# Kernel optimization log

Measured on AMD Instinct MI355X. Metric: run time of the kernel, lower is better.

Reference implementation:

```python
import jax, jax.numpy as jnp
import numpy as np

M, N, E, IN, C, HID, TOPK = 4, 50000, 400000, 128, 128, 256, 2
NEG_SLOPE = 0.2


def setup_inputs() -> dict:
    key = jax.random.key(0)
    k = jax.random.split(key, 16)
    s = lambda f: 1.0 / np.sqrt(f)
    return {
        "x_src": jax.random.normal(k[0], (M, N, IN), jnp.float32),
        "x_dst": jax.random.normal(k[1], (N, IN), jnp.float32),
        "src_idx": jax.random.randint(k[2], (M, E), 0, N),
        "dst_idx": jax.random.randint(k[3], (M, E), 0, N),
        "proj_Ws": jax.random.normal(k[4], (M, IN, C), jnp.float32) * s(IN),
        "proj_bs": jnp.zeros((M, C), jnp.float32),
        "projd_W": jax.random.normal(k[5], (IN, C), jnp.float32) * s(IN),
        "projd_b": jnp.zeros((C,), jnp.float32),
        "lin_src": jax.random.normal(k[6], (M, C), jnp.float32) * s(C),
        "lin_dst": jax.random.normal(k[7], (M, C), jnp.float32) * s(C),
        "gm_W1": jax.random.normal(k[8], (C, C), jnp.float32) * s(C),
        "gm_b1": jnp.zeros((C,), jnp.float32),
        "gm_W2": jax.random.normal(k[9], (C, C), jnp.float32) * s(C),
        "gm_b2": jnp.zeros((C,), jnp.float32),
        "gate_W1": jax.random.normal(k[10], (M * C, HID), jnp.float32) * s(M * C),
        "gate_b1": jnp.zeros((HID,), jnp.float32),
        "gate_W2": jax.random.normal(k[11], (HID, M), jnp.float32) * s(HID),
        "gate_b2": jnp.zeros((M,), jnp.float32),
        "exp_W1": jax.random.normal(k[12], (M, C, HID), jnp.float32) * s(C),
        "exp_b1": jnp.zeros((M, HID), jnp.float32),
        "exp_W2": jax.random.normal(k[13], (M, HID, C), jnp.float32) * s(HID),
        "exp_b2": jnp.zeros((M, C), jnp.float32),
    }


def _propagate(xs_t, asrc_t, adst_t, si, di, recept_t):
    # GAT-style attention message passing for one edge type.
    # xs_t: [N,C] projected src feats, asrc_t/adst_t: [N] attn logits,
    # si/di: [E] edge endpoints, recept_t: [N] per-dst-node receptivity gate.
    e = jax.nn.leaky_relu(asrc_t[si] + adst_t[di], NEG_SLOPE)  # [E]
    emax = jax.ops.segment_max(e, di, num_segments=N)
    ez = jnp.exp(e - emax[di])
    den = jax.ops.segment_sum(ez, di, num_segments=N)
    alpha = ez / (den[di] + 1e-16)                             # softmax per dst node
    msg = xs_t[si] * (alpha * recept_t[di])[:, None]           # [E,C]
    return jax.ops.segment_sum(msg, di, num_segments=N)       # [N,C]


def reference(x_src, x_dst, src_idx, dst_idx, proj_Ws, proj_bs, projd_W, projd_b,
              lin_src, lin_dst, gm_W1, gm_b1, gm_W2, gm_b2,
              gate_W1, gate_b1, gate_W2, gate_b2,
              exp_W1, exp_b1, exp_W2, exp_b2):
    # --- SynapticConvLayer (eval path, heads=1) ---
    xs = jnp.einsum('mni,mic->mnc', x_src, proj_Ws) + proj_bs[:, None, :]  # [M,N,C]
    xd = x_dst @ projd_W + projd_b                                          # [N,C]
    a_src = jnp.einsum('mnc,mc->mn', xs, lin_src)
    a_dst = jnp.einsum('nc,mc->mn', xd[None].repeat(M, 0) * 0 + xd[None], lin_dst) if False else jnp.einsum('nc,mc->mn', xd, lin_dst)
    prop = jax.vmap(_propagate)
    out1 = prop(xs, a_src, a_dst, src_idx, dst_idx, jnp.ones((M, N), xs.dtype))
    # receptivity from grad_map surrogate (inference branch)
    feat_diff = out1 - xd[None]                                            # [M,N,C]
    mo = jax.nn.sigmoid(jax.nn.relu(feat_diff @ gm_W1 + gm_b1) @ gm_W2 + gm_b2)
    gd = (mo * feat_diff).mean(axis=-1)                                    # [M,N]
    recept = gd / (jnp.abs(gd) + 1e-8)                                     # L2-norm over the singleton head dim == abs
    out2 = prop(xs, a_src, a_dst, src_idx, dst_idx, recept)
    feats = jax.nn.relu(out2)                                              # [M,N,C] per-edge-type dst features
    # --- SourceExpertMoE ---
    feats_nm = feats.transpose(1, 0, 2)                                    # [N,M,C]
    gate_in = feats_nm.reshape(N, M * C)
    logits = jax.nn.relu(gate_in @ gate_W1 + gate_b1) @ gate_W2 + gate_b2
    gw = jax.nn.softmax(logits, axis=1)
    scores = gw + recept.T                                                 # gate weights + receptivity
    top_w, top_i = jax.lax.top_k(scores, TOPK)
    top_w = top_w / top_w.sum(axis=1, keepdims=True)
    # expert e applied to source-e features for every node (dense, then gather top-k)
    h = jax.nn.relu(jnp.einsum('nmi,mih->nmh', feats_nm, exp_W1) + exp_b1)
    out_all = jnp.einsum('nmh,mho->nmo', h, exp_W2) + exp_b2               # [N,M,C]
    sel = jnp.take_along_axis(out_all, top_i[:, :, None], axis=1)          # [N,K,C]
    final = (sel * top_w[:, :, None]).sum(axis=1)                          # [N,C]
    return final
```

## Files before the change

kernel.cpp:

```cpp
#include <hip/hip_runtime.h>
#include <hip/hip_bf16.h>
#include <math.h>

#define M_  4
#define N_  50000
#define E_  400000
#define IN_ 128
#define C_  128
#define HID_ 256

template<int AMODE, int EPI, int ASCALE>
__global__ void __launch_bounds__(256) gemm9(
    const float* A, const float* A2, const float* __restrict__ B,
    const float* __restrict__ bias, float* Cmat,
    const int* __restrict__ idx, const int* __restrict__ cnts,
    const float* __restrict__ AS, const float* __restrict__ fdbuf,
    const int* __restrict__ roff,
    int R, int K, int NC,
    long long aBatch, long long bBatch, int biasBatch, long long cBatch,
    long long strideM)
{
  __shared__ float As[2][8][128];
  __shared__ float Bs[2][8][128];
  __shared__ float red[(EPI == 5) ? 128 * 17 : 1];

  const int tid = threadIdx.x;
  const int b = blockIdx.y;
  const int Reff = (AMODE == 4 || AMODE == 5) ? cnts[b] : (cnts ? cnts[0] : R);
  const int rb = blockIdx.x * 128;
  if (rb >= Reff) return;
  const int cb = blockIdx.z * 128;

  const float* Ab = (AMODE == 2) ? A : (A + (long long)b * aBatch);
  const float* Bb = B + (long long)b * bBatch + cb;
  const float* biasb = bias + (long long)b * biasBatch + cb;

  const int ar = tid >> 1;
  const int ak = (tid & 1) * 4;
  const int r_a = rb + ar;
  const bool a_ok = (r_a < Reff);
  long long a_row = 0;
  float a_rs = 0.f;
  if (a_ok) {
    if (AMODE == 4) {
      int orow = idx[(long long)b * N_ + r_a];
      a_row = (long long)orow * K;
      if (ASCALE == 2) a_rs = AS[(long long)b * N_ + orow];
    } else if (AMODE == 5) {
      a_row = (long long)(roff[b] + r_a) * K;
    } else if (AMODE == 2) {
      a_row = (long long)r_a * 128;
    } else {
      a_row = (long long)r_a * K;
    }
  }
  const int bk = tid >> 5;
  const int bc = (tid & 31) * 4;

  const int tx = tid & 15;
  const int ty = tid >> 4;

  float acc[8][8];
  #pragma unroll
  for (int i = 0; i < 8; ++i)
    #pragma unroll
    for (int j = 0; j < 8; ++j) acc[i][j] = 0.f;

  const int nt = K >> 3;
  float4 av = make_float4(0.f, 0.f, 0.f, 0.f), bv;

#define LOAD_TILE(k0)                                                          \
  {                                                                            \
    if (a_ok) {                                                                \
      if (AMODE == 2) {                                                        \
        int kk0 = (k0) + ak;                                                   \
        av = *(const float4*)(Ab + (long long)(kk0 >> 7) * strideM + a_row +   \
                              (kk0 & 127));                                    \
        if (ASCALE == 1) {                                                     \
          float rs = AS[(kk0 >> 7) * N_ + r_a];                                \
          av.x = fmaxf(av.x * rs, 0.f); av.y = fmaxf(av.y * rs, 0.f);          \
          av.z = fmaxf(av.z * rs, 0.f); av.w = fmaxf(av.w * rs, 0.f);          \
        }                                                                      \
      } else {                                                                 \
        av = *(const float4*)(Ab + a_row + (k0) + ak);                         \
        if (AMODE == 1) {                                                      \
          float4 y = *(const float4*)(A2 + (long long)r_a * 128 + (k0) + ak);  \
          av.x -= y.x; av.y -= y.y; av.z -= y.z; av.w -= y.w;                  \
        }                                                                      \
        if (AMODE == 4 && ASCALE == 2) {                                       \
          av.x = fmaxf(av.x * a_rs, 0.f); av.y = fmaxf(av.y * a_rs, 0.f);      \
          av.z = fmaxf(av.z * a_rs, 0.f); av.w = fmaxf(av.w * a_rs, 0.f);      \
        }                                                                      \
      }                                                                        \
    } else {                                                                   \
      av = make_float4(0.f, 0.f, 0.f, 0.f);                                    \
    }                                                                          \
    bv = *(const float4*)(Bb + (long long)((k0) + bk) * NC + bc);              \
  }

#define WRITE_TILE(buf)                                                        \
  {                                                                            \
    As[buf][ak + 0][ar] = av.x; As[buf][ak + 1][ar] = av.y;                    \
    As[buf][ak + 2][ar] = av.z; As[buf][ak + 3][ar] = av.w;                    \
    *(float4*)(&Bs[buf][bk][bc]) = bv;                                         \
  }

  LOAD_TILE(0)
  WRITE_TILE(0)

  for (int t = 0; t < nt; ++t) {
    __syncthreads();
    const int cur = t & 1;
    const bool more = (t + 1 < nt);
    if (more) LOAD_TILE((t + 1) * 8)

    #pragma unroll
    for (int kk = 0; kk < 8; ++kk) {
      float4 alo = *(float4*)(&As[cur][kk][ty * 4]);
      float4 ahi = *(float4*)(&As[cur][kk][64 + ty * 4]);
      float4 blo = *(float4*)(&Bs[cur][kk][tx * 4]);
      float4 bhi = *(float4*)(&Bs[cur][kk][64 + tx * 4]);
      float a8[8] = {alo.x, alo.y, alo.z, alo.w, ahi.x, ahi.y, ahi.z, ahi.w};
      float b8[8] = {blo.x, blo.y, blo.z, blo.w, bhi.x, bhi.y, bhi.z, bhi.w};
      #pragma unroll
      for (int i = 0; i < 8; ++i)
        #pragma unroll
        for (int j = 0; j < 8; ++j)
          acc[i][j] += a8[i] * b8[j];
    }

    if (more) WRITE_TILE(cur ^ 1)
  }
#undef LOAD_TILE
#undef WRITE_TILE

  if (EPI == 5) {
    #pragma unroll
    for (int i = 0; i < 8; ++i) {
      const int r_local = (i < 4 ? ty * 4 + i : 64 + ty * 4 + (i - 4));
      const int r = rb + r_local;
      if (r < Reff) {
        const float* fdrow = fdbuf + (long long)b * cBatch + (long long)r * 128;
        const float* xdrow = A2 + (long long)r * 128;
        float4 flo = *(const float4*)(fdrow + tx * 4);
        float4 fhi = *(const float4*)(fdrow + 64 + tx * 4);
        float4 xlo = *(const float4*)(xdrow + tx * 4);
        float4 xhi = *(const float4*)(xdrow + 64 + tx * 4);
        float fd8[8] = {flo.x - xlo.x, flo.y - xlo.y, flo.z - xlo.z, flo.w - xlo.w,
                        fhi.x - xhi.x, fhi.y - xhi.y, fhi.z - xhi.z, fhi.w - xhi.w};
        float p = 0.f;
        #pragma unroll
        for (int j = 0; j < 8; ++j) {
          const int c = (j < 4 ? tx * 4 + j : 64 + tx * 4 + (j - 4));
          float mo = 1.f / (1.f + expf(-(acc[i][j] + biasb[c])));
          p += mo * fd8[j];
        }
        red[r_local * 17 + tx] = p;
      }
    }
    __syncthreads();
    if (tid < 128) {
      const int r = rb + tid;
      if (r < Reff) {
        float s = 0.f;
        #pragma unroll
        for (int t = 0; t < 16; ++t) s += red[tid * 17 + t];
        float gd = s / 128.f;
        Cmat[(long long)b * N_ + r] = gd / (fabsf(gd) + 1e-8f);
      }
    }
    return;
  }

  #pragma unroll
  for (int i = 0; i < 8; ++i) {
    const int r = rb + (i < 4 ? ty * 4 + i : 64 + ty * 4 + (i - 4));
    if (r >= Reff) continue;
    long long crow;
    if (EPI == 7) crow = (long long)(roff[b] + r) * NC + cb;
    else if (EPI == 9) crow = (long long)(roff[b] + r) * 128 + cb;
    else crow = (long long)b * cBatch + (long long)r * NC + cb;
    #pragma unroll
    for (int j = 0; j < 8; ++j) {
      const int c = (j < 4 ? tx * 4 + j : 64 + tx * 4 + (j - 4));
      float v = acc[i][j] + biasb[c];
      if (EPI == 1 || EPI == 7) v = fmaxf(v, 0.f);
      Cmat[crow + c] = v;
    }
  }
}

__global__ void attn_logit_kernel(const float* __restrict__ X, const float* __restrict__ lin,
                                  float* __restrict__ out, int Nn, int perM)
{
  int m = blockIdx.y;
  int w = blockIdx.x * (blockDim.x >> 6) + (threadIdx.x >> 6);
  int lane = threadIdx.x & 63;
  if (w >= Nn) return;
  long long row = perM ? ((long long)m * Nn + w) : (long long)w;
  const float* xr = X + row * 128;
  const float* lr = lin + m * 128;
  float acc = xr[lane] * lr[lane] + xr[lane + 64] * lr[lane + 64];
  #pragma unroll
  for (int off = 32; off > 0; off >>= 1) acc += __shfl_down(acc, off);
  if (lane == 0) out[(long long)m * Nn + w] = acc;
}

__global__ void count_kernel(const int* __restrict__ dst, int* __restrict__ cnt, int Nn)
{
  int e = blockIdx.x * blockDim.x + threadIdx.x;
  int m = blockIdx.y;
  if (e >= E_) return;
  atomicAdd(&cnt[(long long)m * Nn + dst[(long long)m * E_ + e]], 1);
}

__global__ void chunkscan_kernel(const int* __restrict__ cnt, int* __restrict__ rowptr,
                                 int* __restrict__ chunktot)
{
  int m = blockIdx.y, ch = blockIdx.x;
  int base = ch * 1024;
  const int* c = cnt + (long long)m * N_;
  int* rp = rowptr + (long long)m * (N_ + 1);
  __shared__ int sums[256];
  int t = threadIdx.x;
  int v[4]; int s = 0;
  #pragma unroll
  for (int k = 0; k < 4; ++k) {
    int i = base + t * 4 + k;
    v[k] = (i < N_) ? c[i] : 0;
    s += v[k];
  }
  sums[t] = s;
  __syncthreads();
  for (int off = 1; off < 256; off <<= 1) {
    int x = (t >= off) ? sums[t - off] : 0;
    __syncthreads();
    sums[t] += x;
    __syncthreads();
  }
  int run = sums[t] - s;
  #pragma unroll
  for (int k = 0; k < 4; ++k) {
    int i = base + t * 4 + k;
    run += v[k];
    if (i < N_) rp[i + 1] = run;
  }
  if (t == 255) chunktot[m * 64 + ch] = sums[255];
}

__global__ void scantot_kernel(int* __restrict__ chunktot, int nch)
{
  int m = threadIdx.x;
  if (m >= M_) return;
  int run = 0;
  for (int ch = 0; ch < nch; ++ch) {
    int v = chunktot[m * 64 + ch];
    chunktot[m * 64 + ch] = run;
    run += v;
  }
}

__global__ void addoff_kernel(int* __restrict__ rowptr, const int* __restrict__ chunktot)
{
  int m = blockIdx.y, ch = blockIdx.x;
  int off = chunktot[m * 64 + ch];
  int t = threadIdx.x;
  int* rp = rowptr + (long long)m * (N_ + 1);
  #pragma unroll
  for (int k = 0; k < 4; ++k) {
    int i = ch * 1024 + t * 4 + k;
    if (i < N_) rp[i + 1] += off;
  }
  if (ch == 0 && t == 0) rp[0] = 0;
}

__global__ void scatter_kernel(const int* __restrict__ dst, const int* __restrict__ rowptr,
                               int* __restrict__ fill, int* __restrict__ col, int Nn)
{
  int e = blockIdx.x * blockDim.x + threadIdx.x;
  int m = blockIdx.y;
  if (e >= E_) return;
  int d = dst[(long long)m * E_ + e];
  int pos = rowptr[(long long)m * (Nn + 1) + d] + atomicAdd(&fill[(long long)m * Nn + d], 1);
  col[(long long)m * E_ + pos] = e;
}

__global__ void sortbucket_kernel(const int* __restrict__ rowptr, int* __restrict__ col, int Nn)
{
  int n = blockIdx.x * blockDim.x + threadIdx.x;
  int m = blockIdx.y;
  if (n >= Nn) return;
  const int* rp = rowptr + (long long)m * (Nn + 1);
  int* c = col + (long long)m * E_;
  int b = rp[n], e = rp[n + 1];
  for (int i = b + 1; i < e; ++i) {
    int v = c[i]; int j = i - 1;
    while (j >= b && c[j] > v) { c[j + 1] = c[j]; --j; }
    c[j + 1] = v;
  }
}

__global__ void edge_e_kernel(const int* __restrict__ src, const int* __restrict__ dst,
                              const float* __restrict__ asrc, const float* __restrict__ adst,
                              float* __restrict__ e_edge)
{
  int e = blockIdx.x * blockDim.x + threadIdx.x;
  int m = blockIdx.y;
  if (e >= E_) return;
  long long off = (long long)m * E_ + e;
  float v = asrc[(long long)m * N_ + src[off]] + adst[(long long)m * N_ + dst[off]];
  e_edge[off] = (v >= 0.f) ? v : 0.2f * v;
}

__global__ void alpha_kernel(const int* __restrict__ rowptr, const int* __restrict__ col,
                             const int* __restrict__ src, const float* __restrict__ e_edge,
                             float* __restrict__ alpha, int* __restrict__ src_csr)
{
  int n = blockIdx.x * blockDim.x + threadIdx.x;
  int m = blockIdx.y;
  if (n >= N_) return;
  const int* rp = rowptr + (long long)m * (N_ + 1);
  const int* cl = col + (long long)m * E_;
  const int* sr = src + (long long)m * E_;
  const float* ee = e_edge + (long long)m * E_;
  float* al = alpha + (long long)m * E_;
  int* sc = src_csr + (long long)m * E_;
  int b = rp[n], en = rp[n + 1];
  if (b == en) return;
  float emax = -INFINITY;
  for (int j = b; j < en; ++j) emax = fmaxf(emax, ee[cl[j]]);
  float den = 0.f;
  for (int j = b; j < en; ++j) {
    int eid = cl[j];
    float ez = expf(ee[eid] - emax);
    den += ez;
    al[j] = ez;
    sc[j] = sr[eid];
  }
  float inv = 1.f / (den + 1e-16f);
  for (int j = b; j < en; ++j) al[j] *= inv;
}

__global__ void prop2_kernel(const float* __restrict__ xs, const int* __restrict__ rowptr,
                             const float* __restrict__ alpha, const int* __restrict__ src_csr,
                             float* __restrict__ out)
{
  int d = blockIdx.x * 2 + (threadIdx.x >> 7);
  int m = blockIdx.y;
  int c = threadIdx.x & 127;
  if (d >= N_) return;
  const int* rp = rowptr + (long long)m * (N_ + 1);
  const float* al = alpha + (long long)m * E_;
  const int* sc = src_csr + (long long)m * E_;
  const float* xsm = xs + (long long)m * N_ * 128;
  int b = rp[d], en = rp[d + 1];
  float acc = 0.f;
  int j = b;
  for (; j + 3 < en; j += 4) {
    float a0 = al[j], a1 = al[j + 1], a2 = al[j + 2], a3 = al[j + 3];
    int s0 = sc[j], s1 = sc[j + 1], s2 = sc[j + 2], s3 = sc[j + 3];
    float x0 = xsm[(long long)s0 * 128 + c];
    float x1 = xsm[(long long)s1 * 128 + c];
    float x2 = xsm[(long long)s2 * 128 + c];
    float x3 = xsm[(long long)s3 * 128 + c];
    acc += a0 * x0; acc += a1 * x1; acc += a2 * x2; acc += a3 * x3;
  }
  for (; j < en; ++j)
    acc += al[j] * xsm[(long long)sc[j] * 128 + c];
  out[((long long)m * N_ + d) * 128 + c] = acc;
}

__global__ void gate_logits_kernel(const float* __restrict__ h, const float* __restrict__ W2,
                                   const float* __restrict__ b2, float* __restrict__ logits, int Nn)
{
  int w = blockIdx.x * (blockDim.x >> 6) + (threadIdx.x >> 6);
  int lane = threadIdx.x & 63;
  if (w >= Nn) return;
  const float* hr = h + (long long)w * 256;
  float a0 = 0.f, a1 = 0.f, a2 = 0.f, a3 = 0.f;
  for (int j = lane; j < 256; j += 64) {
    float hv = hr[j];
    a0 += hv * W2[j * 4 + 0];
    a1 += hv * W2[j * 4 + 1];
    a2 += hv * W2[j * 4 + 2];
    a3 += hv * W2[j * 4 + 3];
  }
  #pragma unroll
  for (int off = 32; off > 0; off >>= 1) {
    a0 += __shfl_down(a0, off);
    a1 += __shfl_down(a1, off);
    a2 += __shfl_down(a2, off);
    a3 += __shfl_down(a3, off);
  }
  if (lane == 0) {
    long long o = (long long)w * 4;
    logits[o + 0] = a0 + b2[0];
    logits[o + 1] = a1 + b2[1];
    logits[o + 2] = a2 + b2[2];
    logits[o + 3] = a3 + b2[3];
  }
}

__global__ void topk_kernel(const float* __restrict__ logits, const float* __restrict__ recept,
                            float* __restrict__ wsel, int Nn)
{
  int n = blockIdx.x * blockDim.x + threadIdx.x;
  if (n >= Nn) return;
  float l[4];
  #pragma unroll
  for (int m = 0; m < 4; ++m) l[m] = logits[(long long)n * 4 + m];
  float mx = fmaxf(fmaxf(l[0], l[1]), fmaxf(l[2], l[3]));
  float e[4], s = 0.f;
  #pragma unroll
  for (int m = 0; m < 4; ++m) { e[m] = expf(l[m] - mx); s += e[m]; }
  float sc[4];
  #pragma unroll
  for (int m = 0; m < 4; ++m) sc[m] = e[m] / s + recept[(long long)m * Nn + n];
  int i0 = 0; float v0 = sc[0];
  #pragma unroll
  for (int m = 1; m < 4; ++m) if (sc[m] > v0) { v0 = sc[m]; i0 = m; }
  int i1 = -1; float v1 = -INFINITY;
  #pragma unroll
  for (int m = 0; m < 4; ++m) { if (m == i0) continue; if (sc[m] > v1) { v1 = sc[m]; i1 = m; } }
  float ts = v0 + v1;
  float w0 = v0 / ts, w1 = v1 / ts;
  #pragma unroll
  for (int m = 0; m < 4; ++m)
    wsel[(long long)m * Nn + n] = (m == i0) ? w0 : ((m == i1) ? w1 : 0.f);
}

__global__ void compact_kernel(const float* __restrict__ wsel, int* __restrict__ idx,
                               int* __restrict__ posmn, int* __restrict__ cnts, int Nn)
{
  int n = blockIdx.x * blockDim.x + threadIdx.x;
  if (n >= Nn) return;
  #pragma unroll
  for (int m = 0; m < 4; ++m) {
    if (wsel[(long long)m * Nn + n] != 0.f) {
      int p = atomicAdd(&cnts[m], 1);
      idx[(long long)m * Nn + p] = n;
      posmn[(long long)m * Nn + n] = p;
    }
  }
}

__global__ void prefix4_kernel(const int* __restrict__ cnts, int* __restrict__ off)
{
  if (threadIdx.x == 0) {
    int r = 0;
    #pragma unroll
    for (int m = 0; m < 4; ++m) { off[m] = r; r += cnts[m]; }
  }
}

__global__ void combine_kernel(const float* __restrict__ outp, const float* __restrict__ wsel,
                               const int* __restrict__ posmn, const int* __restrict__ expoff,
                               float* __restrict__ fin)
{
  long long i = (long long)blockIdx.x * blockDim.x + threadIdx.x;
  if (i >= (long long)N_ * 32) return;
  int n = (int)(i >> 5);
  int c4 = (int)(i & 31) * 4;
  float4 acc = make_float4(0.f, 0.f, 0.f, 0.f);
  #pragma unroll
  for (int m = 0; m < 4; ++m) {
    float w = wsel[(long long)m * N_ + n];
    if (w != 0.f) {
      int p = expoff[m] + posmn[(long long)m * N_ + n];
      float4 v = *(const float4*)(outp + (long long)p * 128 + c4);
      acc.x += w * v.x; acc.y += w * v.y; acc.z += w * v.z; acc.w += w * v.w;
    }
  }
  *(float4*)(fin + (long long)n * 128 + c4) = acc;
}

extern "C" void kernel_launch(void* const* d_in, const int* in_sizes, int n_in,
                              void* d_out, int out_size, void* d_ws, size_t ws_size,
                              hipStream_t stream) {
  const float* x_src   = (const float*)d_in[0];
  const float* x_dst   = (const float*)d_in[1];
  const int*   src_idx = (const int*)d_in[2];
  const int*   dst_idx = (const int*)d_in[3];
  const float* proj_Ws = (const float*)d_in[4];
  const float* proj_bs = (const float*)d_in[5];
  const float* projd_W = (const float*)d_in[6];
  const float* projd_b = (const float*)d_in[7];
  const float* lin_src = (const float*)d_in[8];
  const float* lin_dst = (const float*)d_in[9];
  const float* gm_W1   = (const float*)d_in[10];
  const float* gm_b1   = (const float*)d_in[11];
  const float* gm_W2   = (const float*)d_in[12];
  const float* gm_b2   = (const float*)d_in[13];
  const float* gate_W1 = (const float*)d_in[14];
  const float* gate_b1 = (const float*)d_in[15];
  const float* gate_W2 = (const float*)d_in[16];
  const float* gate_b2 = (const float*)d_in[17];
  const float* exp_W1  = (const float*)d_in[18];
  const float* exp_b1  = (const float*)d_in[19];
  const float* exp_W2  = (const float*)d_in[20];
  const float* exp_b2  = (const float*)d_in[21];
  float* final_out = (float*)d_out;

  float* ws = (float*)d_ws;
  float* bufA   = ws;
  float* bufB   = ws + 25600000LL;
  float* xd     = ws + 51200000LL;
  float* asrc   = ws + 57600000LL;
  float* adst   = ws + 57800000LL;
  float* recept = ws + 58000000LL;
  float* wsel   = ws + 58200000LL;
  float* logits = ws + 58400000LL;
  float* e_edge = ws + 58600000LL;
  float* alpha  = ws + 60200000LL;
  int*   ibase  = (int*)(ws + 61800000LL);
  int*   rowptr = ibase;
  int*   col    = ibase + 200004;
  int*   cnt    = ibase + 1800004;
  int*   expidx = cnt;
  int*   expcnt = ibase + 2000004;
  int*   src_csr= ibase + 2000008;
  int*   chunktot = ibase + 3600008;
  int*   expoff = ibase + 3600264;
  int*   posmn  = ibase + 3600268;

  const long long NC = (long long)N_ * C_;
  const int RB = (N_ + 127) / 128;
  const int NCH = (N_ + 1023) / 1024;

  hipMemsetAsync(cnt, 0, (size_t)M_ * N_ * sizeof(int), stream);
  count_kernel<<<dim3((E_ + 255) / 256, M_), 256, 0, stream>>>(dst_idx, cnt, N_);
  chunkscan_kernel<<<dim3(NCH, M_), 256, 0, stream>>>(cnt, rowptr, chunktot);
  scantot_kernel<<<1, 64, 0, stream>>>(chunktot, NCH);
  addoff_kernel<<<dim3(NCH, M_), 256, 0, stream>>>(rowptr, chunktot);
  hipMemsetAsync(cnt, 0, (size_t)M_ * N_ * sizeof(int), stream);
  scatter_kernel<<<dim3((E_ + 255) / 256, M_), 256, 0, stream>>>(dst_idx, rowptr, cnt, col, N_);
  sortbucket_kernel<<<dim3((N_ + 255) / 256, M_), 256, 0, stream>>>(rowptr, col, N_);

  gemm9<0, 0, 0><<<dim3(RB, 1, 1), 256, 0, stream>>>(
      x_dst, nullptr, projd_W, projd_b, xd, nullptr, nullptr, nullptr, nullptr,
      nullptr, N_, IN_, C_, 0, 0, 0, 0, 0);
  attn_logit_kernel<<<dim3((N_ + 3) / 4, M_), 256, 0, stream>>>(xd, lin_dst, adst, N_, 0);

  gemm9<0, 0, 0><<<dim3(RB, M_, 1), 256, 0, stream>>>(
      x_src, nullptr, proj_Ws, proj_bs, bufA, nullptr, nullptr, nullptr, nullptr,
      nullptr, N_, IN_, C_, NC, (long long)IN_ * C_, C_, NC, 0);
  attn_logit_kernel<<<dim3((N_ + 3) / 4, M_), 256, 0, stream>>>(bufA, lin_src, asrc, N_, 1);

  edge_e_kernel<<<dim3((E_ + 255) / 256, M_), 256, 0, stream>>>(
      src_idx, dst_idx, asrc, adst, e_edge);
  alpha_kernel<<<dim3((N_ + 255) / 256, M_), 256, 0, stream>>>(
      rowptr, col, src_idx, e_edge, alpha, src_csr);

  prop2_kernel<<<dim3((N_ + 1) / 2, M_), 256, 0, stream>>>(bufA, rowptr, alpha, src_csr, bufB);

  gemm9<1, 1, 0><<<dim3(RB, M_, 1), 256, 0, stream>>>(
      bufB, xd, gm_W1, gm_b1, bufA, nullptr, nullptr, nullptr, nullptr,
      nullptr, N_, C_, C_, NC, 0, 0, NC, 0);
  gemm9<0, 5, 0><<<dim3(RB, M_, 1), 256, 0, stream>>>(
      bufA, xd, gm_W2, gm_b2, recept, nullptr, nullptr, nullptr, bufB,
      nullptr, N_, C_, C_, NC, 0, 0, NC, 0);

  gemm9<2, 1, 1><<<dim3(RB, 1, 2), 256, 0, stream>>>(
      bufB, nullptr, gate_W1, gate_b1, bufA, nullptr, nullptr, recept, nullptr,
      nullptr, N_, M_ * C_, HID_, 0, 0, 0, 0, NC);
  gate_logits_kernel<<<dim3((N_ + 3) / 4), 256, 0, stream>>>(bufA, gate_W2, gate_b2, logits, N_);
  topk_kernel<<<(N_ + 255) / 256, 256, 0, stream>>>(logits, recept, wsel, N_);

  hipMemsetAsync(expcnt, 0, 4 * sizeof(int), stream);
  compact_kernel<<<(N_ + 255) / 256, 256, 0, stream>>>(wsel, expidx, posmn, expcnt, N_);
  prefix4_kernel<<<1, 64, 0, stream>>>(expcnt, expoff);

  gemm9<4, 7, 2><<<dim3(RB, M_, 2), 256, 0, stream>>>(
      bufB, nullptr, exp_W1, exp_b1, bufA, expidx, expcnt, recept, nullptr,
      expoff, N_, C_, HID_, NC, (long long)C_ * HID_, HID_, 0, 0);
  gemm9<5, 9, 0><<<dim3(RB, M_, 1), 256, 0, stream>>>(
      bufA, nullptr, exp_W2, exp_b2, bufB, expidx, expcnt, nullptr, nullptr,
      expoff, N_, HID_, C_, 0, (long long)HID_ * C_, C_, 0, 0);
  combine_kernel<<<(int)(((long long)N_ * 32 + 255) / 256), 256, 0, stream>>>(
      bufB, wsel, posmn, expoff, final_out);
}
```

Baseline: 1.348 ms.

## Precompute xd@W1 once and single-buffer the GEMM shared-memory tiles

The first gating-MLP GEMM used to compute (out - xd) @ W1 by subtracting xd on every A-tile load for all M edge types. It now computes out @ W1 and subtracts a precomputed xd @ W1, produced once by a new GEMM with a zero bias, in the epilogue. This removes M-1 redundant reads of xd from the inner loop at the cost of one extra GEMM and an extra buffer. Separately, the shared-memory tiles go from double-buffered to single-buffered with two barriers per k-step. That halves LDS use but loses the overlap between tile stores and compute.

Result: faster. 1.290 ms (-4.3%).

```diff
diff --git a/kernel.cpp b/kernel.cpp
--- a/kernel.cpp
+++ b/kernel.cpp
@@ -10,7 +10,7 @@
 #define HID_ 256
 
 template<int AMODE, int EPI, int ASCALE>
-__global__ void __launch_bounds__(256) gemm9(
+__global__ void __launch_bounds__(256) gemm10(
     const float* A, const float* A2, const float* __restrict__ B,
     const float* __restrict__ bias, float* Cmat,
     const int* __restrict__ idx, const int* __restrict__ cnts,
@@ -20,8 +20,8 @@
     long long aBatch, long long bBatch, int biasBatch, long long cBatch,
     long long strideM)
 {
-  __shared__ float As[2][8][128];
-  __shared__ float Bs[2][8][128];
+  __shared__ float As[8][128];
+  __shared__ float Bs[8][128];
   __shared__ float red[(EPI == 5) ? 128 * 17 : 1];
 
   const int tid = threadIdx.x;
@@ -83,10 +83,6 @@
         }                                                                      \
       } else {                                                                 \
         av = *(const float4*)(Ab + a_row + (k0) + ak);                         \
-        if (AMODE == 1) {                                                      \
-          float4 y = *(const float4*)(A2 + (long long)r_a * 128 + (k0) + ak);  \
-          av.x -= y.x; av.y -= y.y; av.z -= y.z; av.w -= y.w;                  \
-        }                                                                      \
         if (AMODE == 4 && ASCALE == 2) {                                       \
           av.x = fmaxf(av.x * a_rs, 0.f); av.y = fmaxf(av.y * a_rs, 0.f);      \
           av.z = fmaxf(av.z * a_rs, 0.f); av.w = fmaxf(av.w * a_rs, 0.f);      \
@@ -98,28 +94,23 @@
     bv = *(const float4*)(Bb + (long long)((k0) + bk) * NC + bc);              \
   }
 
-#define WRITE_TILE(buf)                                                        \
-  {                                                                            \
-    As[buf][ak + 0][ar] = av.x; As[buf][ak + 1][ar] = av.y;                    \
-    As[buf][ak + 2][ar] = av.z; As[buf][ak + 3][ar] = av.w;                    \
-    *(float4*)(&Bs[buf][bk][bc]) = bv;                                         \
-  }
-
   LOAD_TILE(0)
-  WRITE_TILE(0)
 
   for (int t = 0; t < nt; ++t) {
     __syncthreads();
-    const int cur = t & 1;
-    const bool more = (t + 1 < nt);
-    if (more) LOAD_TILE((t + 1) * 8)
+    As[ak + 0][ar] = av.x; As[ak + 1][ar] = av.y;
+    As[ak + 2][ar] = av.z; As[ak + 3][ar] = av.w;
+    *(float4*)(&Bs[bk][bc]) = bv;
+    __syncthreads();
+
+    if (t + 1 < nt) LOAD_TILE((t + 1) * 8)
 
     #pragma unroll
     for (int kk = 0; kk < 8; ++kk) {
-      float4 alo = *(float4*)(&As[cur][kk][ty * 4]);
-      float4 ahi = *(float4*)(&As[cur][kk][64 + ty * 4]);
-      float4 blo = *(float4*)(&Bs[cur][kk][tx * 4]);
-      float4 bhi = *(float4*)(&Bs[cur][kk][64 + tx * 4]);
+      float4 alo = *(float4*)(&As[kk][ty * 4]);
+      float4 ahi = *(float4*)(&As[kk][64 + ty * 4]);
+      float4 blo = *(float4*)(&Bs[kk][tx * 4]);
+      float4 bhi = *(float4*)(&Bs[kk][64 + tx * 4]);
       float a8[8] = {alo.x, alo.y, alo.z, alo.w, ahi.x, ahi.y, ahi.z, ahi.w};
       float b8[8] = {blo.x, blo.y, blo.z, blo.w, bhi.x, bhi.y, bhi.z, bhi.w};
       #pragma unroll
@@ -128,11 +119,8 @@
         for (int j = 0; j < 8; ++j)
           acc[i][j] += a8[i] * b8[j];
     }
-
-    if (more) WRITE_TILE(cur ^ 1)
   }
 #undef LOAD_TILE
-#undef WRITE_TILE
 
   if (EPI == 5) {
     #pragma unroll
@@ -180,10 +168,12 @@
     if (EPI == 7) crow = (long long)(roff[b] + r) * NC + cb;
     else if (EPI == 9) crow = (long long)(roff[b] + r) * 128 + cb;
     else crow = (long long)b * cBatch + (long long)r * NC + cb;
+    const float* subrow = (EPI == 6) ? (fdbuf + (long long)r * 128 + cb) : nullptr;
     #pragma unroll
     for (int j = 0; j < 8; ++j) {
       const int c = (j < 4 ? tx * 4 + j : 64 + tx * 4 + (j - 4));
       float v = acc[i][j] + biasb[c];
+      if (EPI == 6) v = fmaxf(v - subrow[c], 0.f);
       if (EPI == 1 || EPI == 7) v = fmaxf(v, 0.f);
       Cmat[crow + c] = v;
     }
@@ -512,7 +502,9 @@
   float* logits = ws + 58400000LL;
   float* e_edge = ws + 58600000LL;
   float* alpha  = ws + 60200000LL;
-  int*   ibase  = (int*)(ws + 61800000LL);
+  float* xdW1   = ws + 61800000LL;
+  float* zbuf   = ws + 68200000LL;
+  int*   ibase  = (int*)(ws + 68300000LL);
   int*   rowptr = ibase;
   int*   col    = ibase + 200004;
   int*   cnt    = ibase + 1800004;
@@ -528,6 +520,7 @@
   const int NCH = (N_ + 1023) / 1024;
 
   hipMemsetAsync(cnt, 0, (size_t)M_ * N_ * sizeof(int), stream);
+  hipMemsetAsync(zbuf, 0, 128 * sizeof(float), stream);
   count_kernel<<<dim3((E_ + 255) / 256, M_), 256, 0, stream>>>(dst_idx, cnt, N_);
   chunkscan_kernel<<<dim3(NCH, M_), 256, 0, stream>>>(cnt, rowptr, chunktot);
   scantot_kernel<<<1, 64, 0, stream>>>(chunktot, NCH);
@@ -536,12 +529,16 @@
   scatter_kernel<<<dim3((E_ + 255) / 256, M_), 256, 0, stream>>>(dst_idx, rowptr, cnt, col, N_);
   sortbucket_kernel<<<dim3((N_ + 255) / 256, M_), 256, 0, stream>>>(rowptr, col, N_);
 
-  gemm9<0, 0, 0><<<dim3(RB, 1, 1), 256, 0, stream>>>(
+  gemm10<0, 0, 0><<<dim3(RB, 1, 1), 256, 0, stream>>>(
       x_dst, nullptr, projd_W, projd_b, xd, nullptr, nullptr, nullptr, nullptr,
       nullptr, N_, IN_, C_, 0, 0, 0, 0, 0);
   attn_logit_kernel<<<dim3((N_ + 3) / 4, M_), 256, 0, stream>>>(xd, lin_dst, adst, N_, 0);
 
-  gemm9<0, 0, 0><<<dim3(RB, M_, 1), 256, 0, stream>>>(
+  gemm10<0, 0, 0><<<dim3(RB, 1, 1), 256, 0, stream>>>(
+      xd, nullptr, gm_W1, zbuf, xdW1, nullptr, nullptr, nullptr, nullptr,
+      nullptr, N_, C_, C_, 0, 0, 0, 0, 0);
+
+  gemm10<0, 0, 0><<<dim3(RB, M_, 1), 256, 0, stream>>>(
       x_src, nullptr, proj_Ws, proj_bs, bufA, nullptr, nullptr, nullptr, nullptr,
       nullptr, N_, IN_, C_, NC, (long long)IN_ * C_, C_, NC, 0);
   attn_logit_kernel<<<dim3((N_ + 3) / 4, M_), 256, 0, stream>>>(bufA, lin_src, asrc, N_, 1);
@@ -553,14 +550,14 @@
 
   prop2_kernel<<<dim3((N_ + 1) / 2, M_), 256, 0, stream>>>(bufA, rowptr, alpha, src_csr, bufB);
 
-  gemm9<1, 1, 0><<<dim3(RB, M_, 1), 256, 0, stream>>>(
-      bufB, xd, gm_W1, gm_b1, bufA, nullptr, nullptr, nullptr, nullptr,
+  gemm10<0, 6, 0><<<dim3(RB, M_, 1), 256, 0, stream>>>(
+      bufB, nullptr, gm_W1, gm_b1, bufA, nullptr, nullptr, nullptr, xdW1,
       nullptr, N_, C_, C_, NC, 0, 0, NC, 0);
-  gemm9<0, 5, 0><<<dim3(RB, M_, 1), 256, 0, stream>>>(
+  gemm10<0, 5, 0><<<dim3(RB, M_, 1), 256, 0, stream>>>(
       bufA, xd, gm_W2, gm_b2, recept, nullptr, nullptr, nullptr, bufB,
       nullptr, N_, C_, C_, NC, 0, 0, NC, 0);
 
-  gemm9<2, 1, 1><<<dim3(RB, 1, 2), 256, 0, stream>>>(
+  gemm10<2, 1, 1><<<dim3(RB, 1, 2), 256, 0, stream>>>(
       bufB, nullptr, gate_W1, gate_b1, bufA, nullptr, nullptr, recept, nullptr,
       nullptr, N_, M_ * C_, HID_, 0, 0, 0, 0, NC);
   gate_logits_kernel<<<dim3((N_ + 3) / 4), 256, 0, stream>>>(bufA, gate_W2, gate_b2, logits, N_);
@@ -570,10 +567,10 @@
   compact_kernel<<<(N_ + 255) / 256, 256, 0, stream>>>(wsel, expidx, posmn, expcnt, N_);
   prefix4_kernel<<<1, 64, 0, stream>>>(expcnt, expoff);
 
-  gemm9<4, 7, 2><<<dim3(RB, M_, 2), 256, 0, stream>>>(
+  gemm10<4, 7, 2><<<dim3(RB, M_, 2), 256, 0, stream>>>(
       bufB, nullptr, exp_W1, exp_b1, bufA, expidx, expcnt, recept, nullptr,
       expoff, N_, C_, HID_, NC, (long long)C_ * HID_, HID_, 0, 0);
-  gemm9<5, 9, 0><<<dim3(RB, M_, 1), 256, 0, stream>>>(
+  gemm10<5, 9, 0><<<dim3(RB, M_, 1), 256, 0, stream>>>(
       bufA, nullptr, exp_W2, exp_b2, bufB, expidx, expcnt, nullptr, nullptr,
       expoff, N_, HID_, C_, 0, (long long)HID_ * C_, C_, 0, 0);
   combine_kernel<<<(int)(((long long)N_ * 32 + 255) / 256), 256, 0, stream>>>(
```
